# Kernel tuning notes

Measured on AMD Instinct MI355X. Metric: run time of the kernel, lower is better.

## Reference

```python
import jax, jax.numpy as jnp
import numpy as np

N = 4096          # num nodes
D = 128           # feature dim (dataset.x.shape[-1])
E = 131072        # num edges (avg degree 32)
POOL_K = 0.6      # ks[0]
K = max(2, int(POOL_K * N))  # 2457 kept nodes


def setup_inputs() -> dict:
    key = jax.random.key(0)
    ks = jax.random.split(key, 8)
    s = 0.05
    g = jax.random.randint(ks[0], (2, E), 0, N)                      # edge_index
    h = jax.random.normal(ks[1], (N, D), jnp.float32)                # node features
    Wd = jax.random.normal(ks[2], (D, D), jnp.float32) * s           # down-GCN stub
    bd = jnp.zeros((D,), jnp.float32)
    pw = jax.random.normal(ks[3], (D, 1), jnp.float32) * s           # Pool.proj weight
    pb = jnp.zeros((1,), jnp.float32)                                # Pool.proj bias
    Wb = jax.random.normal(ks[4], (D, D), jnp.float32) * s           # bottom-GCN stub
    bb = jnp.zeros((D,), jnp.float32)
    Wu = jax.random.normal(ks[5], (D, D), jnp.float32) * s           # up-GCN stub
    bu = jnp.zeros((D,), jnp.float32)
    return {"g": g, "h": h, "Wd": Wd, "bd": bd, "pw": pw, "pb": pb,
            "Wb": Wb, "bb": bb, "Wu": Wu, "bu": bu}


def reference(g, h, Wd, bd, pw, pb, Wb, bb, Wu, bu):
    dt = h.dtype
    src, dst = g[0], g[1]
    # to_dense_adj: scatter-add edges into dense [N, N] adjacency
    adj = jnp.zeros((N, N), dt).at[src, dst].add(jnp.ones((E,), dt))

    # down GCN (GNNEarly stub, called with h only): linear
    h0 = h @ Wd + bd

    # Pool: score, topk, gather
    scores = jax.nn.sigmoid((h0 @ pw + pb)[:, 0])          # [N]
    values, idx = jax.lax.top_k(scores, K)                 # descending, like torch.topk
    new_h = h0[idx] * values[:, None]                      # [K, D]

    # boolean 2-hop connectivity, then subselect pooled nodes
    un_g = (adj > 0).astype(dt)
    two_hop = ((un_g @ un_g) > 0).astype(dt)               # [N, N]
    sub = two_hop[idx][:, idx]                             # [K, K]
    # norm_g: g / degrees with torch broadcasting => column-normalize by row-degree
    degrees = jnp.sum(sub, axis=1)                         # [K]
    g_p = sub / degrees                                    # sub[i,j] / degrees[j]

    # bottom GCN (stub with pooled graph): propagate + linear
    h_b = g_p @ (new_h @ Wb) + bb                          # [K, D]

    # Unpool: scatter back to N nodes
    h_u = jnp.zeros((N, D), dt).at[idx].set(h_b)

    # up GCN (stub with original dense adj adj_ms[0])
    h_up = adj @ (h_u @ Wu) + bu                           # [N, D]

    h1 = h_up + h0        # h.add(down_outs[0])
    h2 = h1 + h           # h.add(org_h)
    return (h1, h2)       # hs list
```

## Files before the change

### kernel.cpp

```cpp
#include <hip/hip_runtime.h>
#include <hip/hip_bf16.h>
#include <stdint.h>


#define NN 4096
#define DD 128
#define KKEEP 2457
#define SUBW 40
#define MP 2464
#define KP 2560
#define MT 154
#define NT 8
#define KCHUNK (KP / 4)
#define RT 8

typedef unsigned long long u64;
typedef unsigned short ushort_t;
typedef __attribute__((ext_vector_type(8))) short bf16x8;
typedef __attribute__((ext_vector_type(4))) float f32x4;

__global__ void k_zero(float4* __restrict__ p) {
    int i = blockIdx.x * 256 + threadIdx.x;
    p[i] = make_float4(0.f, 0.f, 0.f, 0.f);
}

__global__ void k_h0_build(const float* __restrict__ h, const float* __restrict__ Wd,
                           const float* __restrict__ bd, const float* __restrict__ pw,
                           const float* __restrict__ pb, const int* __restrict__ g, int E,
                           const float* __restrict__ Wb, const float* __restrict__ Wu,
                           const float* __restrict__ bb,
                           float* __restrict__ h0, float* __restrict__ scores,
                           u64* __restrict__ rowbits, int* __restrict__ deg,
                           float* __restrict__ W2, float* __restrict__ cu) {
    __shared__ float rows[RT][DD];
    __shared__ float sred[2][RT];
    int bid = blockIdx.x;
    int d = threadIdx.x;
    if (bid >= 1536) {
        int wb = bid - 1536;
        if (wb < 16) {
            int r0 = wb * RT;
            #pragma unroll
            for (int r = 0; r < RT; ++r) rows[r][d] = Wb[(size_t)(r0 + r) * DD + d];
            __syncthreads();
            float acc[RT];
            #pragma unroll
            for (int r = 0; r < RT; ++r) acc[r] = 0.f;
            for (int kb = 0; kb < DD; kb += 16) {
                float w[16];
                #pragma unroll
                for (int j = 0; j < 16; ++j) w[j] = Wu[(size_t)(kb + j) * DD + d];
                #pragma unroll
                for (int r = 0; r < RT; ++r)
                    #pragma unroll
                    for (int j = 0; j < 16; ++j) acc[r] += rows[r][kb + j] * w[j];
            }
            #pragma unroll
            for (int r = 0; r < RT; ++r) W2[(size_t)(r0 + r) * DD + d] = acc[r];
        } else {
            float a = 0.f;
            for (int m = 0; m < DD; ++m) a += bb[m] * Wu[(size_t)m * DD + d];
            cu[d] = a;
        }
        return;
    }
    if (bid >= 512) {
        int e = (bid - 512) * 128 + d;
        if (e < E) {
            int s = g[e], d2 = g[E + e];
            atomicOr(&rowbits[(size_t)s * 64 + (d2 >> 6)], 1ull << (d2 & 63));
            atomicAdd(&deg[s], 1);
        }
        return;
    }
    int r0 = bid * RT;
    #pragma unroll
    for (int r = 0; r < RT; ++r) rows[r][d] = h[(size_t)(r0 + r) * DD + d];
    __syncthreads();
    float acc[RT];
    float b = bd[d];
    #pragma unroll
    for (int r = 0; r < RT; ++r) acc[r] = b;
    for (int kb = 0; kb < DD; kb += 16) {
        float w[16];
        #pragma unroll
        for (int j = 0; j < 16; ++j) w[j] = Wd[(size_t)(kb + j) * DD + d];
        #pragma unroll
        for (int r = 0; r < RT; ++r)
            #pragma unroll
            for (int j = 0; j < 16; ++j) acc[r] += rows[r][kb + j] * w[j];
    }
    #pragma unroll
    for (int r = 0; r < RT; ++r) h0[(size_t)(r0 + r) * DD + d] = acc[r];
    float pwd = pw[d];
    int lane = d & 63, wv = d >> 6;
    #pragma unroll
    for (int r = 0; r < RT; ++r) {
        float v = acc[r] * pwd;
        #pragma unroll
        for (int s = 32; s > 0; s >>= 1) v += __shfl_xor(v, s);
        if (lane == 0) sred[wv][r] = v;
    }
    __syncthreads();
    if (d < RT) {
        float v = sred[0][d] + sred[1][d];
        scores[r0 + d] = 1.0f / (1.0f + expf(-(v + pb[0])));
    }
}

__global__ void k_rank_scan(const float* __restrict__ scores, const int* __restrict__ deg,
                            int* __restrict__ keep, int* __restrict__ pos,
                            int* __restrict__ idxl, int* __restrict__ off) {
    int bid = blockIdx.x;
    int t = threadIdx.x;
    if (bid == NN / 4) {
        __shared__ int part[256];
        int base = t * 16;
        int loc[16]; int s = 0;
        #pragma unroll
        for (int i = 0; i < 16; ++i) { loc[i] = s; s += deg[base + i]; }
        part[t] = s;
        __syncthreads();
        int sum = 0;
        for (int i = 0; i < t; ++i) sum += part[i];
        #pragma unroll
        for (int i = 0; i < 16; ++i) off[base + i] = sum + loc[i];
        if (t == 255) off[NN] = sum + s;
        return;
    }
    int lane = t & 63;
    int i = bid * 4 + (t >> 6);
    float my = scores[i];
    int rank = 0;
    #pragma unroll 4
    for (int base = 0; base < NN; base += 64) {
        int jj = base + lane;
        float sj = scores[jj];
        u64 m = __ballot((sj > my) || (sj == my && jj < i));
        rank += __popcll(m);
    }
    if (lane == 0) {
        if (rank < KKEEP) { keep[i] = 1; pos[i] = rank; idxl[rank] = i; }
        else keep[i] = 0;
    }
}

__global__ void k_sub_scatter(const u64* __restrict__ rowbits, const int* __restrict__ idxl,
                              const int* __restrict__ g, int E, const int* __restrict__ off,
                              const int* __restrict__ keep, const int* __restrict__ pos,
                              int* __restrict__ cursor, int* __restrict__ csrv,
                              ushort_t* __restrict__ S, float* __restrict__ invdeg) {
    __shared__ int nb[320];
    __shared__ int nbcnt;
    __shared__ int cntS;
    __shared__ u64 accLDS[64];
    int bid = blockIdx.x;
    int t = threadIdx.x;
    if (bid >= MP) {
        int e = (bid - MP) * 256 + t;
        if (e < E) {
            int s = g[e], dd = g[E + e];
            int p = atomicAdd(&cursor[s], 1);
            csrv[off[s] + p] = keep[dd] ? pos[dd] : -1;
        }
        return;
    }
    int r = bid;
    int wv = t >> 6, lane = t & 63;
    ushort_t* Srow = S + (size_t)r * KP;
    if (r >= KKEEP) {
        #pragma unroll
        for (int j = 0; j < 10; ++j) Srow[j * 256 + t] = 0;
        return;
    }
    int i = idxl[r];
    if (wv == 0) {
        u64 rw = rowbits[(size_t)i * 64 + lane];
        int myc = __popcll(rw);
        int pre = myc;
        #pragma unroll
        for (int s2 = 1; s2 < 64; s2 <<= 1) {
            int tt = __shfl_up(pre, s2);
            if (lane >= s2) pre += tt;
        }
        pre -= myc;
        u64 w = rw; int j = 0;
        while (w) {
            int b = __builtin_ctzll(w);
            w &= w - 1;
            nb[pre + j] = lane * 64 + b; ++j;
        }
        if (lane == 63) nbcnt = pre + myc;
    } else if (wv == 1) {
        accLDS[lane] = 0;
    } else if (wv == 2 && lane == 0) {
        cntS = 0;
    }
    __syncthreads();
    int cnt_nb = nbcnt;
    u64 accw = 0;
    for (int j = wv; j < cnt_nb; j += 4)
        accw |= rowbits[(size_t)nb[j] * 64 + lane];
    atomicOr(&accLDS[lane], accw);
    __syncthreads();
    int cntp = 0;
    #pragma unroll
    for (int wjj = 0; wjj < 10; ++wjj) {
        int wj = wv * 10 + wjj;
        int c = wj * 64 + lane;
        int ci = (c < KKEEP) ? idxl[c] : 0;
        u64 w = accLDS[ci >> 6];
        int bit = (c < KKEEP) ? (int)((w >> (ci & 63)) & 1ull) : 0;
        cntp += __popcll(__ballot(bit));
        Srow[c] = bit ? 0x3F80 : 0;
    }
    if (lane == 0) atomicAdd(&cntS, cntp);
    __syncthreads();
    if (t == 0) invdeg[r] = 1.0f / (float)cntS;
}

__global__ void k_t(const float* __restrict__ h0, const float* __restrict__ scores,
                    const int* __restrict__ idxl, const float* __restrict__ W2,
                    const float* __restrict__ invdeg, ushort_t* __restrict__ tT) {
    __shared__ float rows[RT][DD];
    int d = threadIdx.x;
    int r0 = blockIdx.x * RT;
    #pragma unroll
    for (int r = 0; r < RT; ++r) {
        int rr = r0 + r;
        float v = 0.f;
        if (rr < KKEEP) {
            int i = idxl[rr];
            v = h0[(size_t)i * DD + d] * scores[i];
        }
        rows[r][d] = v;
    }
    __syncthreads();
    float acc[RT];
    #pragma unroll
    for (int r = 0; r < RT; ++r) acc[r] = 0.f;
    for (int kb = 0; kb < DD; kb += 16) {
        float w[16];
        #pragma unroll
        for (int j = 0; j < 16; ++j) w[j] = W2[(size_t)(kb + j) * DD + d];
        #pragma unroll
        for (int r = 0; r < RT; ++r)
            #pragma unroll
            for (int j = 0; j < 16; ++j) acc[r] += rows[r][kb + j] * w[j];
    }
    bf16x8 packed;
    #pragma unroll
    for (int r = 0; r < RT; ++r) {
        int rr = r0 + r;
        float v = (rr < KKEEP) ? acc[r] * invdeg[rr] : 0.f;
        __hip_bfloat16 b = __float2bfloat16(v);
        packed[r] = *reinterpret_cast<short*>(&b);
    }
    *reinterpret_cast<bf16x8*>(tT + (size_t)d * KP + r0) = packed;
}

__global__ void k_gemm(const short* __restrict__ S, const short* __restrict__ tT,
                       const float* __restrict__ cu, float* __restrict__ uu) {
    __shared__ f32x4 red[4][64];
    int bid = blockIdx.x;
    int tile = (bid & 7) * (MT * NT / 8) + (bid >> 3);
    int wv = threadIdx.x >> 6, lane = threadIdx.x & 63;
    int rt = tile >> 3, ct = tile & 7;
    const short* arow = S + (size_t)(rt * 16 + (lane & 15)) * KP + ((lane >> 4) * 8) + wv * KCHUNK;
    const short* brow = tT + (size_t)(ct * 16 + (lane & 15)) * KP + ((lane >> 4) * 8) + wv * KCHUNK;
    f32x4 acc = {0.f, 0.f, 0.f, 0.f};
    #pragma unroll 4
    for (int kk = 0; kk < KCHUNK; kk += 32) {
        bf16x8 a = *(const bf16x8*)(arow + kk);
        bf16x8 b = *(const bf16x8*)(brow + kk);
        acc = __builtin_amdgcn_mfma_f32_16x16x32_bf16(a, b, acc, 0, 0, 0);
    }
    red[wv][lane] = acc;
    __syncthreads();
    if (wv == 0) {
        f32x4 s = red[0][lane] + red[1][lane] + red[2][lane] + red[3][lane];
        int col = ct * 16 + (lane & 15);
        float cuv = cu[col];
        int row0 = rt * 16 + ((lane >> 4) * 4);
        #pragma unroll
        for (int j = 0; j < 4; ++j) {
            int row = row0 + j;
            if (row < KKEEP) uu[(size_t)row * DD + col] = s[j] + cuv;
        }
    }
}

__global__ void k_agg(const int* __restrict__ off, const int* __restrict__ csrv,
                      const float* __restrict__ uu, const float* __restrict__ bu,
                      const float* __restrict__ h0, const float* __restrict__ h,
                      float* __restrict__ out) {
    int s = blockIdx.x, d = threadIdx.x;
    int b = off[s], e2 = off[s + 1];
    float acc = 0.f;
    int k = b;
    for (; k + 4 <= e2; k += 4) {
        int v0 = csrv[k], v1 = csrv[k + 1], v2 = csrv[k + 2], v3 = csrv[k + 3];
        float a0 = (v0 >= 0) ? uu[(size_t)v0 * DD + d] : 0.f;
        float a1 = (v1 >= 0) ? uu[(size_t)v1 * DD + d] : 0.f;
        float a2 = (v2 >= 0) ? uu[(size_t)v2 * DD + d] : 0.f;
        float a3 = (v3 >= 0) ? uu[(size_t)v3 * DD + d] : 0.f;
        acc += (a0 + a1) + (a2 + a3);
    }
    for (; k < e2; ++k) {
        int v = csrv[k];
        if (v >= 0) acc += uu[(size_t)v * DD + d];
    }
    size_t o = (size_t)s * DD + d;
    float a = acc + bu[d] + h0[o];
    out[o] = a;
    out[(size_t)NN * DD + o] = a + h[o];
}

extern "C" void kernel_launch(void* const* d_in, const int* in_sizes, int n_in,
                              void* d_out, int out_size, void* d_ws, size_t ws_size,
                              hipStream_t stream) {
    const int*   g  = (const int*)d_in[0];
    const float* h  = (const float*)d_in[1];
    const float* Wd = (const float*)d_in[2];
    const float* bd = (const float*)d_in[3];
    const float* pw = (const float*)d_in[4];
    const float* pb = (const float*)d_in[5];
    const float* Wb = (const float*)d_in[6];
    const float* bb = (const float*)d_in[7];
    const float* Wu = (const float*)d_in[8];
    const float* bu = (const float*)d_in[9];
    float* out = (float*)d_out;
    int E = in_sizes[0] / 2;

    char* ws = (char*)d_ws;
    ushort_t* S       = (ushort_t*)(ws + 0);
    u64*      rowbits = (u64*)  (ws + (13u << 20));
    int*      deg     = (int*)  (ws + (15u << 20));
    int*      cursor  = (int*)  (ws + (15u << 20) + 16384);
    int*      off     = (int*)  (ws + (15u << 20) + 32768);
    float*    h0      = (float*)(ws + (16u << 20));
    ushort_t* tT      = (ushort_t*)(ws + (18u << 20));
    int*      csrv    = (int*)  (ws + (21u << 20));
    float*    uu      = (float*)(ws + (22u << 20));
    float*    scores  = (float*)(ws + (24u << 20));
    float*    invdeg  = (float*)(ws + (24u << 20) + 16384);
    int*      pos     = (int*)  (ws + (24u << 20) + 32768);
    int*      keep    = (int*)  (ws + (24u << 20) + 49152);
    int*      idxl    = (int*)  (ws + (24u << 20) + 65536);
    float*    W2      = (float*)(ws + (24u << 20) + 98304);
    float*    cu      = (float*)(ws + (24u << 20) + 98304 + 65536);

    k_zero<<<520, 256, 0, stream>>>((float4*)rowbits);
    k_h0_build<<<1553, 128, 0, stream>>>(h, Wd, bd, pw, pb, g, E, Wb, Wu, bb,
                                         h0, scores, rowbits, deg, W2, cu);
    k_rank_scan<<<NN / 4 + 1, 256, 0, stream>>>(scores, deg, keep, pos, idxl, off);
    k_sub_scatter<<<MP + E / 256, 256, 0, stream>>>(rowbits, idxl, g, E, off,
                                                    keep, pos, cursor, csrv, S, invdeg);
    k_t<<<KP / RT, DD, 0, stream>>>(h0, scores, idxl, W2, invdeg, tT);
    k_gemm<<<MT * NT, 256, 0, stream>>>((const short*)S, (const short*)tT, cu, uu);
    k_agg<<<NN, DD, 0, stream>>>(off, csrv, uu, bu, h0, h, out);
}
```

Before: 112.5 us.

## Store pooled 2-hop subgraph as bitmask and expand to bf16 via LUT in GEMM

The pooled adjacency matrix S was written as a dense bf16 K×KP matrix (about 12.6 MB) and read back by the MFMA GEMM. Now each row is stored as 40 u64 bitmask words, and the GEMM expands 8 bits at a time into bf16 operands through a 256-entry shared-memory lookup table. A lane shuffle also replaces the LDS read of the accumulated row bits. This removes most of the write and read traffic for S, at the cost of extra LUT construction, a block sync and per-iteration bit extraction in the GEMM inner loop.

```diff
diff --git a/kernel.cpp b/kernel.cpp
--- a/kernel.cpp
+++ b/kernel.cpp
@@ -149,7 +149,7 @@
                               const int* __restrict__ g, int E, const int* __restrict__ off,
                               const int* __restrict__ keep, const int* __restrict__ pos,
                               int* __restrict__ cursor, int* __restrict__ csrv,
-                              ushort_t* __restrict__ S, float* __restrict__ invdeg) {
+                              u64* __restrict__ subbits, float* __restrict__ invdeg) {
     __shared__ int nb[320];
     __shared__ int nbcnt;
     __shared__ int cntS;
@@ -167,10 +167,8 @@
     }
     int r = bid;
     int wv = t >> 6, lane = t & 63;
-    ushort_t* Srow = S + (size_t)r * KP;
     if (r >= KKEEP) {
-        #pragma unroll
-        for (int j = 0; j < 10; ++j) Srow[j * 256 + t] = 0;
+        if (t < SUBW) subbits[(size_t)r * SUBW + t] = 0;
         return;
     }
     int i = idxl[r];
@@ -203,16 +201,18 @@
         accw |= rowbits[(size_t)nb[j] * 64 + lane];
     atomicOr(&accLDS[lane], accw);
     __syncthreads();
+    u64 accw_full = accLDS[lane];
     int cntp = 0;
     #pragma unroll
     for (int wjj = 0; wjj < 10; ++wjj) {
         int wj = wv * 10 + wjj;
         int c = wj * 64 + lane;
         int ci = (c < KKEEP) ? idxl[c] : 0;
-        u64 w = accLDS[ci >> 6];
+        u64 w = __shfl(accw_full, ci >> 6);
         int bit = (c < KKEEP) ? (int)((w >> (ci & 63)) & 1ull) : 0;
-        cntp += __popcll(__ballot(bit));
-        Srow[c] = bit ? 0x3F80 : 0;
+        u64 word = __ballot(bit);
+        cntp += __popcll(word);
+        if (lane == 0) subbits[(size_t)r * SUBW + wj] = word;
     }
     if (lane == 0) atomicAdd(&cntS, cntp);
     __syncthreads();
@@ -259,19 +259,34 @@
     *reinterpret_cast<bf16x8*>(tT + (size_t)d * KP + r0) = packed;
 }
 
-__global__ void k_gemm(const short* __restrict__ S, const short* __restrict__ tT,
+__global__ void k_gemm(const u64* __restrict__ subbits, const short* __restrict__ tT,
                        const float* __restrict__ cu, float* __restrict__ uu) {
     __shared__ f32x4 red[4][64];
+    __shared__ uint4 lut[256];
+    int t = threadIdx.x;
+    {
+        uint32_t x0 = ((t & 1) ? 0x3F80u : 0u) | ((t & 2) ? 0x3F800000u : 0u);
+        uint32_t x1 = ((t & 4) ? 0x3F80u : 0u) | ((t & 8) ? 0x3F800000u : 0u);
+        uint32_t x2 = ((t & 16) ? 0x3F80u : 0u) | ((t & 32) ? 0x3F800000u : 0u);
+        uint32_t x3 = ((t & 64) ? 0x3F80u : 0u) | ((t & 128) ? 0x3F800000u : 0u);
+        lut[t] = make_uint4(x0, x1, x2, x3);
+    }
+    __syncthreads();
     int bid = blockIdx.x;
     int tile = (bid & 7) * (MT * NT / 8) + (bid >> 3);
-    int wv = threadIdx.x >> 6, lane = threadIdx.x & 63;
+    int wv = t >> 6, lane = t & 63;
     int rt = tile >> 3, ct = tile & 7;
-    const short* arow = S + (size_t)(rt * 16 + (lane & 15)) * KP + ((lane >> 4) * 8) + wv * KCHUNK;
+    const u64* abits = subbits + (size_t)(rt * 16 + (lane & 15)) * SUBW;
     const short* brow = tT + (size_t)(ct * 16 + (lane & 15)) * KP + ((lane >> 4) * 8) + wv * KCHUNK;
+    int kbase = wv * KCHUNK + ((lane >> 4) * 8);
     f32x4 acc = {0.f, 0.f, 0.f, 0.f};
     #pragma unroll 4
     for (int kk = 0; kk < KCHUNK; kk += 32) {
-        bf16x8 a = *(const bf16x8*)(arow + kk);
+        int k = kbase + kk;
+        u64 w = abits[k >> 6];
+        int byte = (int)((w >> (k & 63)) & 0xFFull);
+        uint4 af = lut[byte];
+        bf16x8 a = *reinterpret_cast<bf16x8*>(&af);
         bf16x8 b = *(const bf16x8*)(brow + kk);
         acc = __builtin_amdgcn_mfma_f32_16x16x32_bf16(a, b, acc, 0, 0, 0);
     }
@@ -333,7 +348,7 @@
     int E = in_sizes[0] / 2;
 
     char* ws = (char*)d_ws;
-    ushort_t* S       = (ushort_t*)(ws + 0);
+    u64*      subbits = (u64*)  (ws + 0);
     u64*      rowbits = (u64*)  (ws + (13u << 20));
     int*      deg     = (int*)  (ws + (15u << 20));
     int*      cursor  = (int*)  (ws + (15u << 20) + 16384);
@@ -355,8 +370,8 @@
                                          h0, scores, rowbits, deg, W2, cu);
     k_rank_scan<<<NN / 4 + 1, 256, 0, stream>>>(scores, deg, keep, pos, idxl, off);
     k_sub_scatter<<<MP + E / 256, 256, 0, stream>>>(rowbits, idxl, g, E, off,
-                                                    keep, pos, cursor, csrv, S, invdeg);
+                                                    keep, pos, cursor, csrv, subbits, invdeg);
     k_t<<<KP / RT, DD, 0, stream>>>(h0, scores, idxl, W2, invdeg, tT);
-    k_gemm<<<MT * NT, 256, 0, stream>>>((const short*)S, (const short*)tT, cu, uu);
+    k_gemm<<<MT * NT, 256, 0, stream>>>(subbits, (const short*)tT, cu, uu);
     k_agg<<<NN, DD, 0, stream>>>(off, csrv, uu, bu, h0, h, out);
 }
```

New measurement: 107.8 us, median of 2. 4.2% less time.
